# Optimization experiments

Hardware: AMD Instinct MI355X
Metric: run time of the kernel (lower is better)

The kernel has to match this reference:

```python
import jax, jax.numpy as jnp
import numpy as np

HEADS = 8
LATENT = 256
D_HEAD = LATENT // HEADS
SCALE = D_HEAD ** -0.5


def setup_inputs() -> dict:
    key = jax.random.key(0)
    ks = jax.random.split(key, 16)
    Bsz, N, dim_a, dim_b = 2, 2048, 768, 768
    def lin(k, din, dout):
        k1, k2 = jax.random.split(k)
        lim = 1.0 / np.sqrt(din)
        W = jax.random.uniform(k1, (din, dout), jnp.float32, -lim, lim)
        b = jax.random.uniform(k2, (dout,), jnp.float32, -lim, lim)
        return W, b
    Wq_aa, bq_aa = lin(ks[0], dim_a, LATENT)
    Wk_aa, bk_aa = lin(ks[1], dim_a, LATENT)
    Wv_a, bv_a = lin(ks[2], dim_a, LATENT)
    Wk_ab, bk_ab = lin(ks[3], dim_a, LATENT)
    Wq_bb, bq_bb = lin(ks[4], dim_b, LATENT)
    Wo, bo = lin(ks[5], LATENT, LATENT)
    A = jax.random.normal(ks[6], (Bsz, N, dim_a), jnp.float32)
    B = jax.random.normal(ks[7], (Bsz, N, dim_b), jnp.float32)
    return dict(A=A, B=B, Wq_aa=Wq_aa, bq_aa=bq_aa, Wk_aa=Wk_aa, bk_aa=bk_aa,
                Wv_a=Wv_a, bv_a=bv_a, Wk_ab=Wk_ab, bk_ab=bk_ab,
                Wq_bb=Wq_bb, bq_bb=bq_bb, Wo=Wo, bo=bo)


def _split_heads(x):
    Bsz, N, _ = x.shape
    return x.reshape(Bsz, N, HEADS, D_HEAD).transpose(0, 2, 1, 3)  # [B,H,N,d]


def reference(A, B, Wq_aa, bq_aa, Wk_aa, bk_aa, Wv_a, bv_a,
              Wk_ab, bk_ab, Wq_bb, bq_bb, Wo, bo):
    Bsz, N, _ = B.shape
    V = _split_heads(A @ Wv_a + bv_a)
    Q_self = _split_heads(A @ Wq_aa + bq_aa)
    K_self = _split_heads(A @ Wk_aa + bk_aa)
    Q_cross = _split_heads(A @ Wk_ab + bk_ab)
    K_cross = _split_heads(B @ Wq_bb + bq_bb)
    attn_self = jnp.einsum('bhnd,bhmd->bhnm', Q_self, K_self) * SCALE
    attn_cross = jnp.einsum('bhnd,bhmd->bhnm', Q_cross, K_cross) * SCALE
    attn = jax.nn.softmax(attn_self + attn_cross, axis=-1)
    out = jnp.einsum('bhnm,bhmd->bhnd', attn, V)
    out = out.transpose(0, 2, 1, 3).reshape(Bsz, N, LATENT)
    return out @ Wo + bo
```

## Files before the change

kernel.cpp:

```cpp
#include <hip/hip_runtime.h>
#include <hip/hip_bf16.h>
#include <math.h>

#define SCALE  0.17677669529663687f
#define QSCALE 0.25501817444361255f

#if __has_builtin(__builtin_amdgcn_exp2f)
#define EXP2(x) __builtin_amdgcn_exp2f(x)
#else
#define EXP2(x) exp2f(x)
#endif

typedef __attribute__((ext_vector_type(8))) short bf16x8;
typedef __attribute__((ext_vector_type(4))) float f32x4;
typedef unsigned int u32;
typedef unsigned short u16;

#define MFMA16(a, b, c) __builtin_amdgcn_mfma_f32_16x16x32_bf16(a, b, c, 0, 0, 0)

__device__ inline u32 bf16rne(float x) {
    u32 u = __float_as_uint(x);
    return (u + 0x7FFFu + ((u >> 16) & 1u)) >> 16;
}
__device__ inline float bf16tof(u32 h) { return __uint_as_float(h << 16); }
__device__ inline u32 pkbf2(float a, float b) {
    union { __hip_bfloat162 h; u32 u; } cv;
    cv.h = __float22bfloat162_rn(make_float2(a, b));
    return cv.u;
}
__device__ inline int swzb(int row, int b) { return row * 128 + (b ^ ((row & 7) << 4)); }

typedef __attribute__((address_space(1))) const u32 gu32;
typedef __attribute__((address_space(3))) u32 lu32;
#define GL16(g, l) __builtin_amdgcn_global_load_lds((gu32*)(const void*)(g), (lu32*)(void*)(l), 16, 0, 0)

__global__ __launch_bounds__(256) void conv_w(
    const float* __restrict__ W0, const float* __restrict__ W1,
    const float* __restrict__ W2, const float* __restrict__ W3,
    const float* __restrict__ W4, const float* __restrict__ Wo,
    u16* __restrict__ W5t_hi, u16* __restrict__ W5t_lo,
    u16* __restrict__ Wot_hi, u16* __restrict__ Wot_lo)
{
    const int g = blockIdx.z;
    const float* W; int K; u16 *dh, *dl;
    switch (g) {
        case 0: W = W0; K = 768; dh = W5t_hi;              dl = nullptr;  break;
        case 1: W = W1; K = 768; dh = W5t_hi + 196608;     dl = nullptr;  break;
        case 2: W = W2; K = 768; dh = W5t_hi + 2 * 196608; dl = nullptr;  break;
        case 3: W = W3; K = 768; dh = W5t_hi + 3 * 196608; dl = nullptr;  break;
        case 4: W = W4; K = 768; dh = W5t_hi + 4 * 196608; dl = nullptr;  break;
        default: W = Wo; K = 256; dh = Wot_hi; dl = Wot_lo; break;
    }
    (void)W5t_lo;
    const int k0 = blockIdx.x * 64, n0 = blockIdx.y * 64;
    if (k0 >= K) return;
    __shared__ float T[64][65];
    const int t = threadIdx.x;
    #pragma unroll
    for (int rep = 0; rep < 4; ++rep) {
        int kr = rep * 16 + (t >> 4);
        int nc = (t & 15) * 4;
        float4 f = *(const float4*)&W[(size_t)(k0 + kr) * 256 + n0 + nc];
        T[kr][nc] = f.x; T[kr][nc + 1] = f.y; T[kr][nc + 2] = f.z; T[kr][nc + 3] = f.w;
    }
    __syncthreads();
    #pragma unroll
    for (int rep = 0; rep < 4; ++rep) {
        int idx = rep * 256 + t;
        int n = idx >> 4, kq = (idx & 15) * 4;
        float v0 = T[kq + 0][n], v1 = T[kq + 1][n], v2 = T[kq + 2][n], v3 = T[kq + 3][n];
        u32 h0 = bf16rne(v0), h1 = bf16rne(v1), h2 = bf16rne(v2), h3 = bf16rne(v3);
        ushort4 hv = {(u16)h0, (u16)h1, (u16)h2, (u16)h3};
        size_t o = (size_t)(n0 + n) * K + k0 + kq;
        *(ushort4*)&dh[o] = hv;
        if (dl) {
            ushort4 lv = {(u16)bf16rne(v0 - bf16tof(h0)), (u16)bf16rne(v1 - bf16tof(h1)),
                          (u16)bf16rne(v2 - bf16tof(h2)), (u16)bf16rne(v3 - bf16tof(h3))};
            *(ushort4*)&dl[o] = lv;
        }
    }
}

__global__ __launch_bounds__(256, 3) void proj_fused(
    const float* __restrict__ A, const float* __restrict__ Bm,
    const u16* __restrict__ W5t_hi,
    const float* __restrict__ b0, const float* __restrict__ b1,
    const float* __restrict__ b2, const float* __restrict__ b3,
    const float* __restrict__ b4,
    u16* __restrict__ Qpk_hi, u16* __restrict__ Qpk_lo,
    u16* __restrict__ Kpk_hi, u16* __restrict__ Vt_hi)
{
    __shared__ u16 XH[64 * 64], XL[64 * 64];
    __shared__ u16 WB[2][128 * 64];

    const int t = threadIdx.x, w = t >> 6, l = t & 63;
    const int l15 = l & 15, lg = l >> 4;

    const int i = blockIdx.x;
    const int v = (i & 7) * 80 + (i >> 3);
    const int unit = v % 10;
    const int g = unit >> 1;
    const int half = unit & 1;
    const int bm = (v / 10) * 64;

    const float* X = (g == 4) ? Bm : A;
    const u16* Wh = W5t_hi + (size_t)g * 196608 + (size_t)half * 98304;
    const float* bias;
    switch (g) {
        case 0: bias = b0; break;
        case 1: bias = b1; break;
        case 2: bias = b2; break;
        case 3: bias = b3; break;
        default: bias = b4; break;
    }
    const bool isq = (g == 0 || g == 3);

    const int lr = l >> 3;
    const int wswz = ((l & 7) * 16) ^ ((lr & 7) << 4);
    const u16* whp = Wh + (size_t)lr * 768 + (wswz >> 1);

    const int xr = t >> 2;
    const float* xp = X + (size_t)(bm + xr) * 768 + (t & 3) * 16;
    const int xb0 = swzb(xr, (t & 3) * 32);
    const int xb1 = swzb(xr, (t & 3) * 32 + 16);

    f32x4 acc[8];
    #pragma unroll
    for (int cg = 0; cg < 8; ++cg) acc[cg] = (f32x4){0.f, 0.f, 0.f, 0.f};

    float4 fc0, fc1, fc2, fc3;
    auto load_x = [&]() {
        fc0 = ((const float4*)xp)[0]; fc1 = ((const float4*)xp)[1];
        fc2 = ((const float4*)xp)[2]; fc3 = ((const float4*)xp)[3];
        xp += 64;
    };
    auto convert_x = [&]() {
        float va[16] = {fc0.x, fc0.y, fc0.z, fc0.w, fc1.x, fc1.y, fc1.z, fc1.w,
                        fc2.x, fc2.y, fc2.z, fc2.w, fc3.x, fc3.y, fc3.z, fc3.w};
        u32 hp[8], lp[8];
        #pragma unroll
        for (int jj = 0; jj < 8; ++jj) {
            float a = va[2 * jj], bq = va[2 * jj + 1];
            u32 hq = pkbf2(a, bq);
            hp[jj] = hq;
            lp[jj] = pkbf2(a - bf16tof(hq & 0xffffu), bq - bf16tof(hq >> 16));
        }
        uint4 u;
        u.x = hp[0]; u.y = hp[1]; u.z = hp[2]; u.w = hp[3];
        *(uint4*)((char*)XH + xb0) = u;
        u.x = hp[4]; u.y = hp[5]; u.z = hp[6]; u.w = hp[7];
        *(uint4*)((char*)XH + xb1) = u;
        u.x = lp[0]; u.y = lp[1]; u.z = lp[2]; u.w = lp[3];
        *(uint4*)((char*)XL + xb0) = u;
        u.x = lp[4]; u.y = lp[5]; u.z = lp[6]; u.w = lp[7];
        *(uint4*)((char*)XL + xb1) = u;
    };
    auto stage_w = [&](u16* buf) {
        #pragma unroll
        for (int j = 0; j < 4; ++j) {
            int c = w * 4 + j;
            GL16(whp + (size_t)c * 6144, &buf[c * 512]);
        }
        whp += 64;
    };

    load_x();
    stage_w(WB[0]);
    convert_x();
    load_x();

    for (int ks = 0; ks < 12; ++ks) {
        __syncthreads();
        if (ks < 11) stage_w(WB[(ks + 1) & 1]);

        const char* Wc = (const char*)WB[ks & 1];
        #pragma unroll
        for (int s = 0; s < 2; ++s) {
            int byo = s * 64 + lg * 16;
            bf16x8 ah = *(const bf16x8*)((const char*)XH + swzb(w * 16 + l15, byo));
            bf16x8 al = *(const bf16x8*)((const char*)XL + swzb(w * 16 + l15, byo));
            #pragma unroll
            for (int cg = 0; cg < 8; ++cg) {
                bf16x8 bh = *(const bf16x8*)(Wc + swzb(cg * 16 + l15, byo));
                acc[cg] = MFMA16(ah, bh, acc[cg]);
                acc[cg] = MFMA16(al, bh, acc[cg]);
            }
        }

        if (ks < 11) {
            convert_x();
            if (ks < 10) load_x();
        }
    }

    float biasv[8];
    #pragma unroll
    for (int cg = 0; cg < 8; ++cg) biasv[cg] = bias[half * 128 + cg * 16 + l15];

    if (g != 2) {
        u16* Dh = isq ? Qpk_hi : Kpk_hi;
        const int dofs = (g == 3 || g == 4) ? 32 : 0;
        #pragma unroll
        for (int cg = 0; cg < 8; ++cg) {
            int c = half * 128 + cg * 16 + l15;
            int h = c >> 5, d = (c & 31) + dofs;
            #pragma unroll
            for (int r = 0; r < 4; ++r) {
                int row = bm + w * 16 + lg * 4 + r;
                float y = acc[cg][r] + biasv[cg];
                if (isq) y *= QSCALE;
                u32 hb = bf16rne(y);
                size_t o = ((size_t)row * 8 + h) * 64 + d;
                Dh[o] = (u16)hb;
                if (isq) Qpk_lo[o] = (u16)bf16rne(y - bf16tof(hb));
            }
        }
    } else {
        __syncthreads();
        #pragma unroll
        for (int cg = 0; cg < 8; ++cg) {
            int dl = cg * 16 + l15;
            #pragma unroll
            for (int r = 0; r < 4; ++r) {
                int kl = w * 16 + lg * 4 + r;
                float y = acc[cg][r] + biasv[cg];
                int byo = (2 * kl) ^ ((dl & 7) << 4);
                *(u16*)((char*)WB[0] + dl * 128 + byo) = (u16)bf16rne(y);
            }
        }
        __syncthreads();
        const int bb = bm >> 11, kb = bm & 2047;
        #pragma unroll
        for (int rep = 0; rep < 8; ++rep) {
            int idx = rep * 256 + t;
            int dl = idx >> 4;
            int kq = idx & 15;
            int dg = half * 128 + dl;
            int h = dg >> 5, d = dg & 31;
            int byo = (8 * kq) ^ ((dl & 7) << 4);
            ushort4 hv = *(const ushort4*)((const char*)WB[0] + dl * 128 + byo);
            size_t o = (((size_t)bb * 8 + h) * 32 + d) * 2048 + kb + kq * 4;
            *(ushort4*)&Vt_hi[o] = hv;
        }
    }
}

__global__ __launch_bounds__(256, 4) void attn_mfma8(
    const u16* __restrict__ Qpk_hi, const u16* __restrict__ Qpk_lo,
    const u16* __restrict__ Kpk_hi, const u16* __restrict__ Vt_hi,
    float* __restrict__ Opart, float* __restrict__ Oml)
{
    __shared__ u16 KH[2][64 * 64], VH[2][32 * 64];
    __shared__ u16 PH[4][16 * 64];

    const int t = threadIdx.x, w = t >> 6, l = t & 63;
    const int l15 = l & 15, lg = l >> 4;

    const int i = blockIdx.x;
    const int v = (i & 7) * 128 + (i >> 3);
    const int panel = v >> 5;
    const int qb   = v & 31;
    const int h = panel >> 2;
    const int z = panel & 3;
    const int b = z >> 1, ks = z & 1;
    const int q0 = qb * 64 + w * 16;
    const int base = b * 2048;

    bf16x8 qh[2], ql[2];
    {
        size_t ro = ((size_t)(base + q0 + l15) * 8 + h) * 64;
        #pragma unroll
        for (int s = 0; s < 2; ++s) {
            qh[s] = *(const bf16x8*)&Qpk_hi[ro + s * 32 + lg * 8];
            ql[s] = *(const bf16x8*)&Qpk_lo[ro + s * 32 + lg * 8];
        }
    }

    const u16* sp[3]; int sstep[3];
    u16* dp0[3]; u16* dp1[3];
    {
        const int k00 = ks * 1024;
        #pragma unroll
        for (int i2 = 0; i2 < 3; ++i2) {
            int c = w + i2 * 4;
            if (c < 8) {
                int r0 = c * 8, r = r0 + (l >> 3);
                int swz = ((l & 7) * 16) ^ ((r & 7) << 4);
                sp[i2] = Kpk_hi + ((size_t)(base + k00 + r) * 8 + h) * 64 + (swz >> 1);
                sstep[i2] = 32768;
                dp0[i2] = &KH[0][r0 * 64];
                dp1[i2] = &KH[1][r0 * 64];
            } else {
                int r0 = (c - 8) * 8, r = r0 + (l >> 3);
                int swz = ((l & 7) * 16) ^ ((r & 7) << 4);
                sp[i2] = Vt_hi + (((size_t)b * 8 + h) * 32 + r) * 2048 + k00 + (swz >> 1);
                sstep[i2] = 64;
                dp0[i2] = &VH[0][r0 * 64];
                dp1[i2] = &VH[1][r0 * 64];
            }
        }
    }

    auto stage = [&](u16* const (&dpx)[3]) {
        #pragma unroll
        for (int i2 = 0; i2 < 3; ++i2) { GL16(sp[i2], dpx[i2]); sp[i2] += sstep[i2]; }
    };

    float m_i = -INFINITY, l_i = 0.f;
    f32x4 o0 = {0.f, 0.f, 0.f, 0.f}, o1 = {0.f, 0.f, 0.f, 0.f};

    auto compute_tile = [&](const u16* KHc, const u16* VHc) {
        f32x4 ta[4] = {{0.f,0.f,0.f,0.f},{0.f,0.f,0.f,0.f},{0.f,0.f,0.f,0.f},{0.f,0.f,0.f,0.f}};
        #pragma unroll
        for (int s = 0; s < 2; ++s) {
            int byo = s * 64 + lg * 16;
            #pragma unroll
            for (int cj = 0; cj < 4; ++cj) {
                bf16x8 kh = *(const bf16x8*)((const char*)KHc + swzb(cj * 16 + l15, byo));
                ta[cj] = MFMA16(kh, qh[s], ta[cj]);
                ta[cj] = MFMA16(kh, ql[s], ta[cj]);
            }
        }

        float t0 = fmaxf(fmaxf(ta[0][0], ta[0][1]), fmaxf(ta[0][2], ta[0][3]));
        float t1 = fmaxf(fmaxf(ta[1][0], ta[1][1]), fmaxf(ta[1][2], ta[1][3]));
        float t2 = fmaxf(fmaxf(ta[2][0], ta[2][1]), fmaxf(ta[2][2], ta[2][3]));
        float t3 = fmaxf(fmaxf(ta[3][0], ta[3][1]), fmaxf(ta[3][2], ta[3][3]));
        float tmax = fmaxf(fmaxf(t0, t1), fmaxf(t2, t3));
        tmax = fmaxf(tmax, __shfl_xor(tmax, 16));
        tmax = fmaxf(tmax, __shfl_xor(tmax, 32));
        if (!__all(tmax <= m_i + 8.0f)) {
            float mnew = fmaxf(m_i, tmax);
            float sc = EXP2(m_i - mnew);
            l_i *= sc;
            #pragma unroll
            for (int r = 0; r < 4; ++r) {
                float fac = __shfl(sc, lg * 4 + r);
                o0[r] *= fac;
                o1[r] *= fac;
            }
            m_i = mnew;
        }
        #pragma unroll
        for (int cj = 0; cj < 4; ++cj)
            #pragma unroll
            for (int r = 0; r < 4; ++r)
                ta[cj][r] = EXP2(ta[cj][r] - m_i);
        float s0 = (ta[0][0] + ta[0][1]) + (ta[0][2] + ta[0][3]);
        float s1 = (ta[1][0] + ta[1][1]) + (ta[1][2] + ta[1][3]);
        float s2 = (ta[2][0] + ta[2][1]) + (ta[2][2] + ta[2][3]);
        float s3 = (ta[3][0] + ta[3][1]) + (ta[3][2] + ta[3][3]);
        float tsum = (s0 + s1) + (s2 + s3);
        tsum += __shfl_xor(tsum, 16);
        tsum += __shfl_xor(tsum, 32);
        l_i += tsum;

        #pragma unroll
        for (int cj = 0; cj < 4; ++cj) {
            uint2 pv = {pkbf2(ta[cj][0], ta[cj][1]), pkbf2(ta[cj][2], ta[cj][3])};
            *(uint2*)((char*)PH[w] + swzb(l15, cj * 32 + lg * 8)) = pv;
        }

        #pragma unroll
        for (int kq = 0; kq < 2; ++kq) {
            int byo = kq * 64 + lg * 16;
            bf16x8 pa  = *(const bf16x8*)((const char*)PH[w] + swzb(l15, byo));
            bf16x8 vh0 = *(const bf16x8*)((const char*)VHc + swzb(l15, byo));
            bf16x8 vh1 = *(const bf16x8*)((const char*)VHc + swzb(16 + l15, byo));
            o0 = MFMA16(pa, vh0, o0);
            o1 = MFMA16(pa, vh1, o1);
        }
    };

    stage(dp0);
    #pragma unroll 1
    for (int it2 = 0; it2 < 8; ++it2) {
        __syncthreads();
        stage(dp1);
        compute_tile(KH[0], VH[0]);
        __syncthreads();
        if (it2 < 7) stage(dp0);
        compute_tile(KH[1], VH[1]);
    }

    const int pb = (b * 8 + h) * 2 + ks;
    #pragma unroll
    for (int r = 0; r < 4; ++r) {
        int row = q0 + lg * 4 + r;
        size_t ob = ((size_t)pb * 2048 + row) * 32;
        Opart[ob + l15]      = o0[r];
        Opart[ob + 16 + l15] = o1[r];
    }
    if (l < 16) {
        int row = q0 + l15;
        float2 ml = {m_i, l_i};
        *(float2*)&Oml[((size_t)pb * 2048 + row) * 2] = ml;
    }
}

__global__ __launch_bounds__(256) void attn_merge(
    const float* __restrict__ Opart, const float* __restrict__ Oml,
    u16* __restrict__ Cx_hi, u16* __restrict__ Cx_lo)
{
    const int t = threadIdx.x;
    const int d = t & 31, rg = t >> 5;
    const int h = blockIdx.y, b = blockIdx.z;
    const int pb = (b * 8 + h) * 2;
    #pragma unroll
    for (int rr = 0; rr < 4; ++rr) {
        int row = blockIdx.x * 32 + rr * 8 + rg;
        float m[2], lv[2];
        #pragma unroll
        for (int i = 0; i < 2; ++i) {
            size_t mb = ((size_t)(pb + i) * 2048 + row) * 2;
            m[i]  = Oml[mb];
            lv[i] = Oml[mb + 1];
        }
        float M = fmaxf(m[0], m[1]);
        float w0 = exp2f(m[0] - M), w1 = exp2f(m[1] - M);
        float L = lv[0] * w0 + lv[1] * w1;
        float o = w0 * Opart[((size_t)pb * 2048 + row) * 32 + d]
                + w1 * Opart[((size_t)(pb + 1) * 2048 + row) * 32 + d];
        float y = o / L;
        u32 hb = bf16rne(y);
        size_t orow = (size_t)(b * 2048 + row) * 256 + h * 32 + d;
        Cx_hi[orow] = (u16)hb;
        Cx_lo[orow] = (u16)bf16rne(y - bf16tof(hb));
    }
}

__global__ __launch_bounds__(256, 2) void gemm_out_mfma(
    const u16* __restrict__ Xhi, const u16* __restrict__ Xlo,
    const u16* __restrict__ Wth, const u16* __restrict__ Wtl,
    const float* __restrict__ bias, float* __restrict__ out)
{
    __shared__ u16 XH[64 * 64], XL[64 * 64], WH[64 * 64], WL[64 * 64];
    const int t = threadIdx.x, w = t >> 6, l = t & 63;
    const int l15 = l & 15, lg = l >> 4;
    const int bn = blockIdx.x * 64, bm = blockIdx.y * 64;

    const u16* srole = (w == 0) ? Xhi : (w == 1) ? Xlo : (w == 2) ? Wth : Wtl;
    u16* drole = (w == 0) ? XH : (w == 1) ? XL : (w == 2) ? WH : WL;
    const int rbase = (w < 2) ? bm : bn;

    const u16* sp[8];
    #pragma unroll
    for (int c = 0; c < 8; ++c) {
        int r = c * 8 + (l >> 3);
        int swz = ((l & 7) * 16) ^ ((r & 7) << 4);
        sp[c] = srole + (size_t)(rbase + r) * 256 + (swz >> 1);
    }

    f32x4 acc[4] = {{0.f,0.f,0.f,0.f},{0.f,0.f,0.f,0.f},{0.f,0.f,0.f,0.f},{0.f,0.f,0.f,0.f}};

    for (int k0 = 0; k0 < 256; k0 += 64) {
        __syncthreads();
        #pragma unroll
        for (int c = 0; c < 8; ++c) { GL16(sp[c], &drole[c * 512]); sp[c] += 64; }
        __syncthreads();
        #pragma unroll
        for (int s = 0; s < 2; ++s) {
            int byo = s * 64 + lg * 16;
            bf16x8 ah = *(const bf16x8*)((const char*)XH + swzb(w * 16 + l15, byo));
            bf16x8 al = *(const bf16x8*)((const char*)XL + swzb(w * 16 + l15, byo));
            #pragma unroll
            for (int cj = 0; cj < 4; ++cj) {
                bf16x8 bh = *(const bf16x8*)((const char*)WH + swzb(cj * 16 + l15, byo));
                bf16x8 bl = *(const bf16x8*)((const char*)WL + swzb(cj * 16 + l15, byo));
                acc[cj] = MFMA16(ah, bh, acc[cj]);
                acc[cj] = MFMA16(al, bh, acc[cj]);
                acc[cj] = MFMA16(ah, bl, acc[cj]);
            }
        }
    }

    #pragma unroll
    for (int cj = 0; cj < 4; ++cj) {
        float bv = bias[bn + cj * 16 + l15];
        #pragma unroll
        for (int r = 0; r < 4; ++r) {
            int row = bm + w * 16 + lg * 4 + r;
            out[(size_t)row * 256 + bn + cj * 16 + l15] = acc[cj][r] + bv;
        }
    }
}

extern "C" void kernel_launch(void* const* d_in, const int* in_sizes, int n_in,
                              void* d_out, int out_size, void* d_ws, size_t ws_size,
                              hipStream_t stream) {
    const float* A     = (const float*)d_in[0];
    const float* B     = (const float*)d_in[1];
    const float* Wq_aa = (const float*)d_in[2];
    const float* bq_aa = (const float*)d_in[3];
    const float* Wk_aa = (const float*)d_in[4];
    const float* bk_aa = (const float*)d_in[5];
    const float* Wv_a  = (const float*)d_in[6];
    const float* bv_a  = (const float*)d_in[7];
    const float* Wk_ab = (const float*)d_in[8];
    const float* bk_ab = (const float*)d_in[9];
    const float* Wq_bb = (const float*)d_in[10];
    const float* bq_bb = (const float*)d_in[11];
    const float* Wo    = (const float*)d_in[12];
    const float* bo    = (const float*)d_in[13];
    float* out = (float*)d_out;

    char* p = (char*)d_ws;
    u16* spare0 = (u16*)p; p += 6291456;
    u16* spare1 = (u16*)p; p += 6291456;
    u16* spare2 = (u16*)p; p += 6291456;
    u16* spare3 = (u16*)p; p += 6291456;
    u16* W5t_hi = (u16*)p; p += 1966080;
    u16* W5t_lo = (u16*)p; p += 1966080;
    u16* Wot_hi = (u16*)p; p += 131072;
    u16* Wot_lo = (u16*)p; p += 131072;
    u16* Qpk_hi = (u16*)p; p += 4194304;
    u16* Qpk_lo = (u16*)p; p += 4194304;
    u16* Kpk_hi = (u16*)p; p += 4194304;
    u16* Kpk_lo = (u16*)p; p += 4194304;
    u16* Vt_hi  = (u16*)p; p += 2097152;
    u16* Vt_lo  = (u16*)p; p += 2097152;
    u16* Cx_hi  = (u16*)p; p += 2097152;
    u16* Cx_lo  = (u16*)p; p += 2097152;
    (void)spare0; (void)spare1; (void)spare2; (void)spare3;
    (void)Kpk_lo; (void)Vt_lo;

    float* Opart = (float*)d_ws;
    float* Oml   = (float*)((char*)d_ws + 8388608);

    conv_w<<<dim3(12, 4, 6), 256, 0, stream>>>(Wq_aa, Wk_aa, Wv_a, Wk_ab, Wq_bb, Wo,
                                               W5t_hi, W5t_lo, Wot_hi, Wot_lo);
    proj_fused<<<dim3(640), 256, 0, stream>>>(A, B, W5t_hi,
                                              bq_aa, bk_aa, bv_a, bk_ab, bq_bb,
                                              Qpk_hi, Qpk_lo, Kpk_hi, Vt_hi);
    attn_mfma8<<<dim3(1024), 256, 0, stream>>>(Qpk_hi, Qpk_lo, Kpk_hi, Vt_hi,
                                               Opart, Oml);
    attn_merge<<<dim3(64, 8, 2), 256, 0, stream>>>(Opart, Oml, Cx_hi, Cx_lo);
    gemm_out_mfma<<<dim3(4, 64), 256, 0, stream>>>(Cx_hi, Cx_lo, Wot_hi, Wot_lo, bo, out);
}
```

Baseline: 78.90 us.

## Fuse split-K attention merge into output GEMM and add MFMA priority hints

After: 80.18 us. Within noise of the previous version (+1.6%).

```diff
diff --git a/kernel.cpp b/kernel.cpp
--- a/kernel.cpp
+++ b/kernel.cpp
@@ -311,6 +311,7 @@
 
     auto compute_tile = [&](const u16* KHc, const u16* VHc) {
         f32x4 ta[4] = {{0.f,0.f,0.f,0.f},{0.f,0.f,0.f,0.f},{0.f,0.f,0.f,0.f},{0.f,0.f,0.f,0.f}};
+        __builtin_amdgcn_s_setprio(1);
         #pragma unroll
         for (int s = 0; s < 2; ++s) {
             int byo = s * 64 + lg * 16;
@@ -321,6 +322,7 @@
                 ta[cj] = MFMA16(kh, ql[s], ta[cj]);
             }
         }
+        __builtin_amdgcn_s_setprio(0);
 
         float t0 = fmaxf(fmaxf(ta[0][0], ta[0][1]), fmaxf(ta[0][2], ta[0][3]));
         float t1 = fmaxf(fmaxf(ta[1][0], ta[1][1]), fmaxf(ta[1][2], ta[1][3]));
@@ -361,6 +363,7 @@
             *(uint2*)((char*)PH[w] + swzb(l15, cj * 32 + lg * 8)) = pv;
         }
 
+        __builtin_amdgcn_s_setprio(1);
         #pragma unroll
         for (int kq = 0; kq < 2; ++kq) {
             int byo = kq * 64 + lg * 16;
@@ -370,6 +373,7 @@
             o0 = MFMA16(pa, vh0, o0);
             o1 = MFMA16(pa, vh1, o1);
         }
+        __builtin_amdgcn_s_setprio(0);
     };
 
     stage(dp0);
@@ -398,66 +402,98 @@
     }
 }
 
-__global__ __launch_bounds__(256) void attn_merge(
+__global__ __launch_bounds__(256, 2) void gemm_out_fused(
     const float* __restrict__ Opart, const float* __restrict__ Oml,
-    u16* __restrict__ Cx_hi, u16* __restrict__ Cx_lo)
-{
-    const int t = threadIdx.x;
-    const int d = t & 31, rg = t >> 5;
-    const int h = blockIdx.y, b = blockIdx.z;
-    const int pb = (b * 8 + h) * 2;
-    #pragma unroll
-    for (int rr = 0; rr < 4; ++rr) {
-        int row = blockIdx.x * 32 + rr * 8 + rg;
-        float m[2], lv[2];
-        #pragma unroll
-        for (int i = 0; i < 2; ++i) {
-            size_t mb = ((size_t)(pb + i) * 2048 + row) * 2;
-            m[i]  = Oml[mb];
-            lv[i] = Oml[mb + 1];
-        }
-        float M = fmaxf(m[0], m[1]);
-        float w0 = exp2f(m[0] - M), w1 = exp2f(m[1] - M);
-        float L = lv[0] * w0 + lv[1] * w1;
-        float o = w0 * Opart[((size_t)pb * 2048 + row) * 32 + d]
-                + w1 * Opart[((size_t)(pb + 1) * 2048 + row) * 32 + d];
-        float y = o / L;
-        u32 hb = bf16rne(y);
-        size_t orow = (size_t)(b * 2048 + row) * 256 + h * 32 + d;
-        Cx_hi[orow] = (u16)hb;
-        Cx_lo[orow] = (u16)bf16rne(y - bf16tof(hb));
-    }
-}
-
-__global__ __launch_bounds__(256, 2) void gemm_out_mfma(
-    const u16* __restrict__ Xhi, const u16* __restrict__ Xlo,
     const u16* __restrict__ Wth, const u16* __restrict__ Wtl,
     const float* __restrict__ bias, float* __restrict__ out)
 {
-    __shared__ u16 XH[64 * 64], XL[64 * 64], WH[64 * 64], WL[64 * 64];
+    __shared__ u16 XH[64 * 64], XL[64 * 64];
+    __shared__ u16 WHB[2][64 * 64], WLB[2][64 * 64];
+
     const int t = threadIdx.x, w = t >> 6, l = t & 63;
     const int l15 = l & 15, lg = l >> 4;
     const int bn = blockIdx.x * 64, bm = blockIdx.y * 64;
-
-    const u16* srole = (w == 0) ? Xhi : (w == 1) ? Xlo : (w == 2) ? Wth : Wtl;
-    u16* drole = (w == 0) ? XH : (w == 1) ? XL : (w == 2) ? WH : WL;
-    const int rbase = (w < 2) ? bm : bn;
-
-    const u16* sp[8];
-    #pragma unroll
-    for (int c = 0; c < 8; ++c) {
-        int r = c * 8 + (l >> 3);
-        int swz = ((l & 7) * 16) ^ ((r & 7) << 4);
-        sp[c] = srole + (size_t)(rbase + r) * 256 + (swz >> 1);
-    }
+    const int bb = bm >> 11;
+
+    const int lr = l >> 3;
+    const int wswz = ((l & 7) * 16) ^ ((lr & 7) << 4);
+    const u16* whp = Wth + (size_t)(bn + lr) * 256 + (wswz >> 1);
+    const u16* wlp = Wtl + (size_t)(bn + lr) * 256 + (wswz >> 1);
+
+    const int xr = t >> 2;
+    const int grl = (bm & 2047) + xr;
+    const int hloc = (t >> 1) & 1;
+    const int d0 = (t & 1) * 16;
+    const int xb0 = swzb(xr, (t & 3) * 32);
+    const int xb1 = swzb(xr, (t & 3) * 32 + 16);
 
     f32x4 acc[4] = {{0.f,0.f,0.f,0.f},{0.f,0.f,0.f,0.f},{0.f,0.f,0.f,0.f},{0.f,0.f,0.f,0.f}};
 
-    for (int k0 = 0; k0 < 256; k0 += 64) {
+    float4 op0[4], op1[4];
+    float2 ml0, ml1;
+    auto load_ctx = [&](int kstep) {
+        int hh = kstep * 2 + hloc;
+        size_t pb = ((size_t)(bb * 8 + hh)) * 2;
+        const float* p0 = &Opart[(pb * 2048 + grl) * 32 + d0];
+        const float* p1 = &Opart[((pb + 1) * 2048 + grl) * 32 + d0];
+        #pragma unroll
+        for (int j = 0; j < 4; ++j) { op0[j] = ((const float4*)p0)[j]; op1[j] = ((const float4*)p1)[j]; }
+        ml0 = *(const float2*)&Oml[(pb * 2048 + grl) * 2];
+        ml1 = *(const float2*)&Oml[((pb + 1) * 2048 + grl) * 2];
+    };
+    auto convert_ctx = [&]() {
+        float M = fmaxf(ml0.x, ml1.x);
+        float w0 = exp2f(ml0.x - M), w1 = exp2f(ml1.x - M);
+        float L = ml0.y * w0 + ml1.y * w1;
+        float a0 = w0 / L, a1 = w1 / L;
+        float y[16];
+        #pragma unroll
+        for (int j = 0; j < 4; ++j) {
+            y[4 * j + 0] = a0 * op0[j].x + a1 * op1[j].x;
+            y[4 * j + 1] = a0 * op0[j].y + a1 * op1[j].y;
+            y[4 * j + 2] = a0 * op0[j].z + a1 * op1[j].z;
+            y[4 * j + 3] = a0 * op0[j].w + a1 * op1[j].w;
+        }
+        u32 hp[8], lp[8];
+        #pragma unroll
+        for (int jj = 0; jj < 8; ++jj) {
+            float a = y[2 * jj], bq = y[2 * jj + 1];
+            u32 hq = pkbf2(a, bq);
+            hp[jj] = hq;
+            lp[jj] = pkbf2(a - bf16tof(hq & 0xffffu), bq - bf16tof(hq >> 16));
+        }
+        uint4 u;
+        u.x = hp[0]; u.y = hp[1]; u.z = hp[2]; u.w = hp[3];
+        *(uint4*)((char*)XH + xb0) = u;
+        u.x = hp[4]; u.y = hp[5]; u.z = hp[6]; u.w = hp[7];
+        *(uint4*)((char*)XH + xb1) = u;
+        u.x = lp[0]; u.y = lp[1]; u.z = lp[2]; u.w = lp[3];
+        *(uint4*)((char*)XL + xb0) = u;
+        u.x = lp[4]; u.y = lp[5]; u.z = lp[6]; u.w = lp[7];
+        *(uint4*)((char*)XL + xb1) = u;
+    };
+    auto stage_w = [&](int buf) {
+        #pragma unroll
+        for (int j = 0; j < 4; ++j) {
+            int c = w * 4 + j;
+            if (c < 8) GL16(whp + (size_t)c * 2048, &WHB[buf][c * 512]);
+            else       GL16(wlp + (size_t)(c - 8) * 2048, &WLB[buf][(c - 8) * 512]);
+        }
+        whp += 64; wlp += 64;
+    };
+
+    load_ctx(0);
+    stage_w(0);
+    convert_ctx();
+    load_ctx(1);
+
+    #pragma unroll
+    for (int ks = 0; ks < 4; ++ks) {
         __syncthreads();
-        #pragma unroll
-        for (int c = 0; c < 8; ++c) { GL16(sp[c], &drole[c * 512]); sp[c] += 64; }
-        __syncthreads();
+        if (ks < 3) stage_w((ks + 1) & 1);
+
+        const char* Wh = (const char*)WHB[ks & 1];
+        const char* Wl = (const char*)WLB[ks & 1];
         #pragma unroll
         for (int s = 0; s < 2; ++s) {
             int byo = s * 64 + lg * 16;
@@ -465,12 +501,17 @@
             bf16x8 al = *(const bf16x8*)((const char*)XL + swzb(w * 16 + l15, byo));
             #pragma unroll
             for (int cj = 0; cj < 4; ++cj) {
-                bf16x8 bh = *(const bf16x8*)((const char*)WH + swzb(cj * 16 + l15, byo));
-                bf16x8 bl = *(const bf16x8*)((const char*)WL + swzb(cj * 16 + l15, byo));
+                bf16x8 bh = *(const bf16x8*)(Wh + swzb(cj * 16 + l15, byo));
+                bf16x8 bl = *(const bf16x8*)(Wl + swzb(cj * 16 + l15, byo));
                 acc[cj] = MFMA16(ah, bh, acc[cj]);
                 acc[cj] = MFMA16(al, bh, acc[cj]);
                 acc[cj] = MFMA16(ah, bl, acc[cj]);
             }
+        }
+
+        if (ks < 3) {
+            convert_ctx();
+            if (ks < 2) load_ctx(ks + 2);
         }
     }
 
@@ -522,7 +563,7 @@
     u16* Cx_hi  = (u16*)p; p += 2097152;
     u16* Cx_lo  = (u16*)p; p += 2097152;
     (void)spare0; (void)spare1; (void)spare2; (void)spare3;
-    (void)Kpk_lo; (void)Vt_lo;
+    (void)Kpk_lo; (void)Vt_lo; (void)Cx_hi; (void)Cx_lo;
 
     float* Opart = (float*)d_ws;
     float* Oml   = (float*)((char*)d_ws + 8388608);
@@ -534,6 +575,6 @@
                                               Qpk_hi, Qpk_lo, Kpk_hi, Vt_hi);
     attn_mfma8<<<dim3(1024), 256, 0, stream>>>(Qpk_hi, Qpk_lo, Kpk_hi, Vt_hi,
                                                Opart, Oml);
-    attn_merge<<<dim3(64, 8, 2), 256, 0, stream>>>(Opart, Oml, Cx_hi, Cx_lo);
-    gemm_out_mfma<<<dim3(4, 64), 256, 0, stream>>>(Cx_hi, Cx_lo, Wot_hi, Wot_lo, bo, out);
-}
+    gemm_out_fused<<<dim3(4, 64), 256, 0, stream>>>(Opart, Oml, Wot_hi, Wot_lo,
+                                                    bo, out);
+}
```
